# Performance work log

Hardware: AMD Instinct MI355X
Metric: run time of the kernel (lower is better)

The kernel has to match this reference:

```python
import jax, jax.numpy as jnp
import numpy as np

N, M, D = 16384, 1024, 1024


def setup_inputs() -> dict:
    key = jax.random.key(0)
    kq, kp = jax.random.split(key)
    query = jax.random.normal(kq, (N, D), dtype=jnp.float32)
    proto = jax.random.normal(kp, (M, D), dtype=jnp.float32)
    return {"query": query, "proto": proto}


def reference(query, proto):
    # Pairwise squared euclidean: ||q||^2 - 2 q.p + ||p||^2  (same math as
    # the expand+pow+sum in compute_euclidean, but without the [N,M,D] blowup).
    q2 = jnp.sum(query * query, axis=-1, keepdims=True)          # [N,1]
    p2 = jnp.sum(proto * proto, axis=-1)                          # [M]
    qp = jnp.einsum('nd,md->nm', query, proto)                    # [N,M]
    dists = q2 - 2.0 * qp + p2[None, :]                           # [N,M]
    # Original applies F.softmax(-dists, dim=1) (named log_p_y but is softmax).
    return jax.nn.softmax(-dists, axis=1)
```

## Files before the change

kernel.cpp:

```cpp
#include <hip/hip_runtime.h>
#include <stdint.h>

#define N_Q 16384
#define M_P 1024
#define D_K 1024

typedef __attribute__((ext_vector_type(8))) __bf16 bf16x8;
typedef __attribute__((ext_vector_type(4))) float floatx4;
typedef __attribute__((ext_vector_type(4))) unsigned int uint4v;

#define AS1 __attribute__((address_space(1)))
#define AS3 __attribute__((address_space(3)))

__device__ __forceinline__ unsigned short f2bf(float f) {
    unsigned int u = __float_as_uint(f);
    u += 0x7fffu + ((u >> 16) & 1u);
    return (unsigned short)(u >> 16);
}
__device__ __forceinline__ float bf2f(unsigned short h) {
    return __uint_as_float(((unsigned int)h) << 16);
}

__device__ __forceinline__ void split_chunk(floatx4 f0, floatx4 f1,
                                            uint4v* hi, uint4v* lo) {
    float e[8] = {f0.x, f0.y, f0.z, f0.w, f1.x, f1.y, f1.z, f1.w};
    unsigned int hb[4], lb[4];
#pragma unroll
    for (int p = 0; p < 4; ++p) {
        unsigned int u0 = __float_as_uint(e[2 * p]);
        unsigned int u1 = __float_as_uint(e[2 * p + 1]);
        hb[p] = __builtin_amdgcn_perm(u1, u0, 0x07060302);
        float l0 = e[2 * p]     - __uint_as_float(u0 & 0xffff0000u);
        float l1 = e[2 * p + 1] - __uint_as_float(u1 & 0xffff0000u);
        lb[p] = __builtin_amdgcn_perm(__float_as_uint(l1), __float_as_uint(l0),
                                      0x07060302);
    }
    uint4v h = {hb[0], hb[1], hb[2], hb[3]};
    uint4v l = {lb[0], lb[1], lb[2], lb[3]};
    *hi = h;
    *lo = l;
}

__global__ __launch_bounds__(256) void convert_proto_kernel(
    const float* __restrict__ proto, unsigned short* __restrict__ ph,
    unsigned short* __restrict__ pl, float* __restrict__ p2) {
    __shared__ float sred[4];
    int m = blockIdx.x;
    int t = threadIdx.x;
    size_t base4 = (size_t)m * (D_K / 4) + t;
    float4 v = ((const float4*)proto)[base4];
    ushort4 h, l;
    h.x = f2bf(v.x); l.x = f2bf(v.x - bf2f(h.x));
    h.y = f2bf(v.y); l.y = f2bf(v.y - bf2f(h.y));
    h.z = f2bf(v.z); l.z = f2bf(v.z - bf2f(h.z));
    h.w = f2bf(v.w); l.w = f2bf(v.w - bf2f(h.w));
    ((ushort4*)ph)[base4] = h;
    ((ushort4*)pl)[base4] = l;
    float sq = v.x * v.x + v.y * v.y + v.z * v.z + v.w * v.w;
#pragma unroll
    for (int off = 1; off < 64; off <<= 1) sq += __shfl_xor(sq, off);
    if ((t & 63) == 0) sred[t >> 6] = sq;
    __syncthreads();
    if (t == 0) p2[m] = sred[0] + sred[1] + sred[2] + sred[3];
}

__global__ __launch_bounds__(128, 2) void gemm_logits_kernel(
    const float* __restrict__ query,
    const unsigned short* __restrict__ ph, const unsigned short* __restrict__ pl,
    const float* __restrict__ p2, float* __restrict__ out) {
    __shared__ unsigned short sAh[128 * 32];
    __shared__ unsigned short sAl[128 * 32];
    __shared__ unsigned short sBh[128 * 32];
    __shared__ unsigned short sBl[128 * 32];

    const int tid = threadIdx.x;
    const int wave = tid >> 6;
    const int lane = tid & 63;
    const int b = blockIdx.x;
    const int mt = (b >> 3) & 7;
    const int nt = (b & 7) | ((b >> 6) << 3);
    const int row0 = nt * 128;
    const int col0 = mt * 128;

    const int rlB = lane >> 2;
    const int cioB = (lane & 3) ^ ((lane >> 3) & 3);
    const size_t laneoffB = (size_t)rlB * D_K + cioB * 8;
    const unsigned short* gB =
        ((wave == 0) ? ph : pl) + (size_t)col0 * D_K + laneoffB;
    unsigned short* dstB = (wave == 0) ? sBh : sBl;

    const int rlA = lane >> 2;
    const int cA = lane & 3;
    const float* gA = query + (size_t)(row0 + wave * 64 + rlA) * D_K + cA * 8;
    const int pw = 4 * rlA + (cA ^ ((rlA >> 1) & 3));
    const int wroff = pw * 8;

    floatx4 zero = {0.0f, 0.0f, 0.0f, 0.0f};
    floatx4 acc[4][8];
#pragma unroll
    for (int i = 0; i < 4; ++i)
#pragma unroll
        for (int j = 0; j < 8; ++j) acc[i][j] = zero;

    const int rsel = lane & 15;
    const int kq = lane >> 4;
    const int gsw = 4 * rsel + (kq ^ ((rsel >> 1) & 3));
    const int fragoff = gsw * 8;

    for (int kt = 0; kt < D_K / 32; ++kt) {
        const int kbase = kt * 32;
#pragma unroll
        for (int s = 0; s < 8; ++s)
            __builtin_amdgcn_global_load_lds(
                (const AS1 unsigned int*)(const void*)(gB + (size_t)(s * 16) * D_K + kbase),
                (AS3 unsigned int*)(void*)(dstB + s * 512), 16, 0, 0);

        floatx4 f0[4], f1[4];
#pragma unroll
        for (int s = 0; s < 4; ++s) {
            const float* p = gA + (size_t)(s * 16) * D_K + kbase;
            f0[s] = *(const floatx4*)p;
            f1[s] = *(const floatx4*)(p + 4);
        }
#pragma unroll
        for (int s = 0; s < 4; ++s) {
            uint4v hi, lo;
            split_chunk(f0[s], f1[s], &hi, &lo);
            const int off = (wave * 4 + s) * 512 + wroff;
            *(uint4v*)(sAh + off) = hi;
            *(uint4v*)(sAl + off) = lo;
        }
        __syncthreads();

        bf16x8 ah[4], al[4];
#pragma unroll
        for (int i = 0; i < 4; ++i) {
            const int aoff = (wave * 4 + i) * 512 + fragoff;
            ah[i] = *(const bf16x8*)(sAh + aoff);
            al[i] = *(const bf16x8*)(sAl + aoff);
        }
#pragma unroll
        for (int j = 0; j < 8; ++j) {
            const int boff = j * 512 + fragoff;
            bf16x8 bhj = *(const bf16x8*)(sBh + boff);
            bf16x8 blj = *(const bf16x8*)(sBl + boff);
#pragma unroll
            for (int i = 0; i < 4; ++i) {
                acc[i][j] = __builtin_amdgcn_mfma_f32_16x16x32_bf16(ah[i], bhj, acc[i][j], 0, 0, 0);
                acc[i][j] = __builtin_amdgcn_mfma_f32_16x16x32_bf16(ah[i], blj, acc[i][j], 0, 0, 0);
                acc[i][j] = __builtin_amdgcn_mfma_f32_16x16x32_bf16(al[i], bhj, acc[i][j], 0, 0, 0);
            }
        }
        __syncthreads();
    }

#pragma unroll
    for (int j = 0; j < 8; ++j) {
        const int gc = col0 + j * 16 + rsel;
        const float p2v = p2[gc];
#pragma unroll
        for (int i = 0; i < 4; ++i) {
            const int gr = row0 + wave * 64 + i * 16 + kq * 4;
#pragma unroll
            for (int r = 0; r < 4; ++r) {
                out[(size_t)(gr + r) * M_P + gc] = 2.0f * acc[i][j][r] - p2v;
            }
        }
    }
}

__global__ __launch_bounds__(256) void naive_logits_kernel(
    const float* __restrict__ query, const float* __restrict__ proto,
    float* __restrict__ out) {
    __shared__ float qs[D_K];
    int n = blockIdx.x;
    int t = threadIdx.x;
    ((float4*)qs)[t] = ((const float4*)(query + (size_t)n * D_K))[t];
    __syncthreads();
    float acc[4] = {0.f, 0.f, 0.f, 0.f};
    float pp[4] = {0.f, 0.f, 0.f, 0.f};
    for (int d = 0; d < D_K; d += 4) {
        float4 qv = *(const float4*)(qs + d);
#pragma unroll
        for (int j = 0; j < 4; ++j) {
            const float4 pv = *(const float4*)(proto + (size_t)(t + 256 * j) * D_K + d);
            acc[j] += qv.x * pv.x + qv.y * pv.y + qv.z * pv.z + qv.w * pv.w;
            pp[j] += pv.x * pv.x + pv.y * pv.y + pv.z * pv.z + pv.w * pv.w;
        }
    }
#pragma unroll
    for (int j = 0; j < 4; ++j)
        out[(size_t)n * M_P + t + 256 * j] = 2.0f * acc[j] - pp[j];
}

__global__ __launch_bounds__(256) void softmax_kernel(float* __restrict__ out) {
    const int lane = threadIdx.x & 63;
    int n = blockIdx.x * 4 + (threadIdx.x >> 6);
    for (int it = 0; it < 2; ++it, n += 8192) {
        float* row = out + (size_t)n * M_P;
        floatx4 v[4];
#pragma unroll
        for (int k = 0; k < 4; ++k)
            v[k] = *((const floatx4*)row + k * 64 + lane);
        float mx = fmaxf(fmaxf(v[0].x, v[0].y), fmaxf(v[0].z, v[0].w));
#pragma unroll
        for (int k = 1; k < 4; ++k)
            mx = fmaxf(mx, fmaxf(fmaxf(v[k].x, v[k].y), fmaxf(v[k].z, v[k].w)));
#pragma unroll
        for (int off = 1; off < 64; off <<= 1) mx = fmaxf(mx, __shfl_xor(mx, off));
        float s = 0.0f;
#pragma unroll
        for (int k = 0; k < 4; ++k) {
            v[k].x = __expf(v[k].x - mx);
            v[k].y = __expf(v[k].y - mx);
            v[k].z = __expf(v[k].z - mx);
            v[k].w = __expf(v[k].w - mx);
            s += v[k].x + v[k].y + v[k].z + v[k].w;
        }
#pragma unroll
        for (int off = 1; off < 64; off <<= 1) s += __shfl_xor(s, off);
        const float inv = 1.0f / s;
#pragma unroll
        for (int k = 0; k < 4; ++k) {
            floatx4 o;
            o.x = v[k].x * inv; o.y = v[k].y * inv;
            o.z = v[k].z * inv; o.w = v[k].w * inv;
            __builtin_nontemporal_store(o, (floatx4*)row + k * 64 + lane);
        }
    }
}

extern "C" void kernel_launch(void* const* d_in, const int* in_sizes, int n_in,
                              void* d_out, int out_size, void* d_ws, size_t ws_size,
                              hipStream_t stream) {
    const float* query = (const float*)d_in[0];
    const float* proto = (const float*)d_in[1];
    float* out = (float*)d_out;

    const size_t pElems = (size_t)M_P * D_K;
    const size_t needed = pElems * 2 * 2 + M_P * 4;

    if (ws_size >= needed) {
        unsigned short* ph = (unsigned short*)d_ws;
        unsigned short* pl = ph + pElems;
        float* p2 = (float*)(pl + pElems);

        convert_proto_kernel<<<M_P, 256, 0, stream>>>(proto, ph, pl, p2);
        gemm_logits_kernel<<<(N_Q / 128) * (M_P / 128), 128, 0, stream>>>(
            query, ph, pl, p2, out);
    } else {
        naive_logits_kernel<<<N_Q, 256, 0, stream>>>(query, proto, out);
    }
    softmax_kernel<<<2048, 256, 0, stream>>>(out);
}
```

Baseline: 214.4 us.

## Double-buffer LDS tiles and split GEMM block across four waves

The GEMM block grows from two waves to four, arranged as a 2x2 grid that each compute a 64x64 sub-tile, so each wave holds half the accumulators it held before. LDS tiles for the A and B halves are double-buffered. The next k-slice's global loads and its bf16 split into shared memory are issued around the MFMA work on the current buffer, leaving one barrier per step. This aims to hide global-load latency behind MFMA work and raise occupancy, at the cost of twice the LDS footprint.

```diff
diff --git a/kernel.cpp b/kernel.cpp
--- a/kernel.cpp
+++ b/kernel.cpp
@@ -64,18 +64,20 @@
     if (t == 0) p2[m] = sred[0] + sred[1] + sred[2] + sred[3];
 }
 
-__global__ __launch_bounds__(128, 2) void gemm_logits_kernel(
+__global__ __launch_bounds__(256, 2) void gemm_logits_kernel(
     const float* __restrict__ query,
     const unsigned short* __restrict__ ph, const unsigned short* __restrict__ pl,
     const float* __restrict__ p2, float* __restrict__ out) {
-    __shared__ unsigned short sAh[128 * 32];
-    __shared__ unsigned short sAl[128 * 32];
-    __shared__ unsigned short sBh[128 * 32];
-    __shared__ unsigned short sBl[128 * 32];
+    __shared__ unsigned short sAh[2][128 * 32];
+    __shared__ unsigned short sAl[2][128 * 32];
+    __shared__ unsigned short sBh[2][128 * 32];
+    __shared__ unsigned short sBl[2][128 * 32];
 
     const int tid = threadIdx.x;
     const int wave = tid >> 6;
     const int lane = tid & 63;
+    const int wr = wave >> 1;
+    const int wc = wave & 1;
     const int b = blockIdx.x;
     const int mt = (b >> 3) & 7;
     const int nt = (b & 7) | ((b >> 6) << 3);
@@ -84,66 +86,68 @@
 
     const int rlB = lane >> 2;
     const int cioB = (lane & 3) ^ ((lane >> 3) & 3);
-    const size_t laneoffB = (size_t)rlB * D_K + cioB * 8;
-    const unsigned short* gB =
-        ((wave == 0) ? ph : pl) + (size_t)col0 * D_K + laneoffB;
-    unsigned short* dstB = (wave == 0) ? sBh : sBl;
+    const int halfB = wave & 1;
+    const int sgrpB = wave >> 1;
+    const unsigned short* gB = (halfB ? pl : ph)
+        + (size_t)(col0 + sgrpB * 64 + rlB) * D_K + cioB * 8;
 
     const int rlA = lane >> 2;
     const int cA = lane & 3;
-    const float* gA = query + (size_t)(row0 + wave * 64 + rlA) * D_K + cA * 8;
-    const int pw = 4 * rlA + (cA ^ ((rlA >> 1) & 3));
-    const int wroff = pw * 8;
-
-    floatx4 zero = {0.0f, 0.0f, 0.0f, 0.0f};
-    floatx4 acc[4][8];
-#pragma unroll
-    for (int i = 0; i < 4; ++i)
-#pragma unroll
-        for (int j = 0; j < 8; ++j) acc[i][j] = zero;
+    const float* gA = query + (size_t)(row0 + wave * 32 + rlA) * D_K + cA * 8;
+    const int wroff = (4 * rlA + (cA ^ ((rlA >> 1) & 3))) * 8;
 
     const int rsel = lane & 15;
     const int kq = lane >> 4;
-    const int gsw = 4 * rsel + (kq ^ ((rsel >> 1) & 3));
-    const int fragoff = gsw * 8;
-
-    for (int kt = 0; kt < D_K / 32; ++kt) {
-        const int kbase = kt * 32;
-#pragma unroll
-        for (int s = 0; s < 8; ++s)
-            __builtin_amdgcn_global_load_lds(
-                (const AS1 unsigned int*)(const void*)(gB + (size_t)(s * 16) * D_K + kbase),
-                (AS3 unsigned int*)(void*)(dstB + s * 512), 16, 0, 0);
-
-        floatx4 f0[4], f1[4];
-#pragma unroll
-        for (int s = 0; s < 4; ++s) {
-            const float* p = gA + (size_t)(s * 16) * D_K + kbase;
+    const int fragoff = (4 * rsel + (kq ^ ((rsel >> 1) & 3))) * 8;
+
+    floatx4 zero = {0.0f, 0.0f, 0.0f, 0.0f};
+    floatx4 acc[4][4];
+#pragma unroll
+    for (int i = 0; i < 4; ++i)
+#pragma unroll
+        for (int j = 0; j < 4; ++j) acc[i][j] = zero;
+
+    floatx4 f0[2], f1[2];
+
+    auto issueA = [&](int kb) {
+#pragma unroll
+        for (int s = 0; s < 2; ++s) {
+            const float* p = gA + (size_t)(s * 16) * D_K + kb;
             f0[s] = *(const floatx4*)p;
             f1[s] = *(const floatx4*)(p + 4);
         }
-#pragma unroll
-        for (int s = 0; s < 4; ++s) {
+    };
+    auto issueB = [&](int kb, int buf) {
+        unsigned short* dstB = halfB ? sBl[buf] : sBh[buf];
+#pragma unroll
+        for (int s = 0; s < 4; ++s)
+            __builtin_amdgcn_global_load_lds(
+                (const AS1 unsigned int*)(const void*)(gB + (size_t)(s * 16) * D_K + kb),
+                (AS3 unsigned int*)(void*)(dstB + (sgrpB * 4 + s) * 512), 16, 0, 0);
+    };
+    auto writeA = [&](int buf) {
+#pragma unroll
+        for (int s = 0; s < 2; ++s) {
             uint4v hi, lo;
             split_chunk(f0[s], f1[s], &hi, &lo);
-            const int off = (wave * 4 + s) * 512 + wroff;
-            *(uint4v*)(sAh + off) = hi;
-            *(uint4v*)(sAl + off) = lo;
-        }
-        __syncthreads();
-
+            const int off = (wave * 2 + s) * 512 + wroff;
+            *(uint4v*)(sAh[buf] + off) = hi;
+            *(uint4v*)(sAl[buf] + off) = lo;
+        }
+    };
+    auto compute = [&](int buf) {
         bf16x8 ah[4], al[4];
 #pragma unroll
         for (int i = 0; i < 4; ++i) {
-            const int aoff = (wave * 4 + i) * 512 + fragoff;
-            ah[i] = *(const bf16x8*)(sAh + aoff);
-            al[i] = *(const bf16x8*)(sAl + aoff);
-        }
-#pragma unroll
-        for (int j = 0; j < 8; ++j) {
-            const int boff = j * 512 + fragoff;
-            bf16x8 bhj = *(const bf16x8*)(sBh + boff);
-            bf16x8 blj = *(const bf16x8*)(sBl + boff);
+            const int aoff = (wr * 4 + i) * 512 + fragoff;
+            ah[i] = *(const bf16x8*)(sAh[buf] + aoff);
+            al[i] = *(const bf16x8*)(sAl[buf] + aoff);
+        }
+#pragma unroll
+        for (int j = 0; j < 4; ++j) {
+            const int boff = (wc * 4 + j) * 512 + fragoff;
+            bf16x8 bhj = *(const bf16x8*)(sBh[buf] + boff);
+            bf16x8 blj = *(const bf16x8*)(sBl[buf] + boff);
 #pragma unroll
             for (int i = 0; i < 4; ++i) {
                 acc[i][j] = __builtin_amdgcn_mfma_f32_16x16x32_bf16(ah[i], bhj, acc[i][j], 0, 0, 0);
@@ -151,16 +155,34 @@
                 acc[i][j] = __builtin_amdgcn_mfma_f32_16x16x32_bf16(al[i], bhj, acc[i][j], 0, 0, 0);
             }
         }
+    };
+    auto step = [&](int kb, int cur, int nxt) {
+        issueA(kb);
+        issueB(kb, nxt);
+        compute(cur);
+        writeA(nxt);
         __syncthreads();
-    }
-
-#pragma unroll
-    for (int j = 0; j < 8; ++j) {
-        const int gc = col0 + j * 16 + rsel;
+    };
+
+    issueA(0);
+    issueB(0, 0);
+    writeA(0);
+    __syncthreads();
+
+    for (int kt = 0; kt < 30; kt += 2) {
+        step((kt + 1) * 32, 0, 1);
+        step((kt + 2) * 32, 1, 0);
+    }
+    step(31 * 32, 0, 1);
+    compute(1);
+
+#pragma unroll
+    for (int j = 0; j < 4; ++j) {
+        const int gc = col0 + wc * 64 + j * 16 + rsel;
         const float p2v = p2[gc];
 #pragma unroll
         for (int i = 0; i < 4; ++i) {
-            const int gr = row0 + wave * 64 + i * 16 + kq * 4;
+            const int gr = row0 + wr * 64 + i * 16 + kq * 4;
 #pragma unroll
             for (int r = 0; r < 4; ++r) {
                 out[(size_t)(gr + r) * M_P + gc] = 2.0f * acc[i][j][r] - p2v;
@@ -246,7 +268,7 @@
         float* p2 = (float*)(pl + pElems);
 
         convert_proto_kernel<<<M_P, 256, 0, stream>>>(proto, ph, pl, p2);
-        gemm_logits_kernel<<<(N_Q / 128) * (M_P / 128), 128, 0, stream>>>(
+        gemm_logits_kernel<<<(N_Q / 128) * (M_P / 128), 256, 0, stream>>>(
             query, ph, pl, p2, out);
     } else {
         naive_logits_kernel<<<N_Q, 256, 0, stream>>>(query, proto, out);
```

After: 250.4 us. +16.8%, slower.
